# Kernel optimization log

Hardware: AMD Instinct MI355X
Metric: run time of the kernel (lower is better)

The kernel has to match this reference:

```python
import jax, jax.numpy as jnp
import numpy as np

B, CIN, COUT, H, W, K = 32, 256, 256, 64, 64, 3


def setup_inputs() -> dict:
    key = jax.random.key(0)
    k1, k2, k3 = jax.random.split(key, 3)
    x = jax.random.normal(k1, (B, CIN, H, W), dtype=jnp.float32)
    # kaiming_uniform_ with a=sqrt(5): bound = sqrt(6 / ((1 + a^2) * fan_in)) = sqrt(1/fan_in)
    fan_in = CIN * K * K
    bound = float(np.sqrt(1.0 / fan_in))
    weight = jax.random.uniform(k2, (COUT, CIN, K, K), dtype=jnp.float32,
                                minval=-bound, maxval=bound)
    bias = jax.random.normal(k3, (COUT,), dtype=jnp.float32)
    return {"x": x, "weight": weight, "bias": bias}


def reference(x, weight, bias):
    # CustomConvnd with kernel=3, stride=1, padding=1 (module doubles it, pad
    # helper splits around center -> 1 element each side, zero padding),
    # equivalent to a standard 2D cross-correlation like torch Conv2d.
    out = jax.lax.conv_general_dilated(
        x, weight,
        window_strides=(1, 1),
        padding=((1, 1), (1, 1)),
        dimension_numbers=("NCHW", "OIHW", "NCHW"),
    )
    return out + bias[None, :, None, None]
```

## Files before the change

kernel.cpp:

```cpp
#include <hip/hip_runtime.h>
#include <hip/hip_bf16.h>

typedef __attribute__((ext_vector_type(8))) short short8;
typedef __attribute__((ext_vector_type(4))) float floatx4;

#define BDIM 512

constexpr int kCIN = 256, kCOUT = 256, kH = 64, kW = 64;
constexpr int BK = 32;
constexpr int NCHUNK = kCIN / BK;
constexpr int XR = 4, XC = 66, NPIX = XR * XC;
constexpr int HW = kH * kW;

__device__ __forceinline__ int swz16(int row, int g) {
    return ((g ^ ((row >> 1) & 3)) << 4);
}

__device__ __forceinline__ unsigned short f2bf(float f) {
    unsigned u = __float_as_uint(f);
    u += 0x7fffu + ((u >> 16) & 1u);
    return (unsigned short)(u >> 16);
}

__global__ void wt_transform_kernel(const float* __restrict__ wsrc,
                                    unsigned short* __restrict__ wt) {
    int idx = blockIdx.x * 256 + threadIdx.x;
    if (idx >= 9 * 256 * 256) return;
    int ci = idx & 255;
    int co = (idx >> 8) & 255;
    int kk = idx >> 16;
    wt[idx] = f2bf(wsrc[(co * 256 + ci) * 9 + kk]);
}

__global__ __launch_bounds__(BDIM)
void conv3x3_mfma_kernel(const float* __restrict__ x,
                         const unsigned short* __restrict__ wt,
                         const float* __restrict__ bias,
                         float* __restrict__ out) {
    __shared__ __align__(16) char xs[NPIX * 64];
    __shared__ __align__(16) char ws[2][256 * 64];

    const int bid = blockIdx.x;
    const int b = bid >> 5;
    const int h0 = (bid & 31) * 2;

    const int tid = threadIdx.x;
    const int wv = tid >> 6;
    const int l = tid & 63;
    const int lo = l & 15;
    const int hi = l >> 4;
    const int co0w = (wv & 3) * 64;
    const int wpix = wv >> 2;

    const float* xb = x + (size_t)b * kCIN * HW;

    floatx4 acc[4][4] = {};

    for (int chunk = 0; chunk < NCHUNK; ++chunk) {
        const int ci0 = chunk * BK;

        for (int t = tid; t < NPIX * 4; t += BDIM) {
            int g = t / NPIX;
            int rem = t - g * NPIX;
            int r = rem / XC;
            int c = rem - r * XC;
            int ih = h0 - 1 + r;
            int iw = c - 1;
            float v[8];
            if ((unsigned)ih < (unsigned)kH && (unsigned)iw < (unsigned)kW) {
                const float* p = xb + (size_t)(ci0 + g * 8) * HW + ih * kW + iw;
                #pragma unroll
                for (int j = 0; j < 8; ++j) v[j] = p[(size_t)j * HW];
            } else {
                #pragma unroll
                for (int j = 0; j < 8; ++j) v[j] = 0.f;
            }
            union { short8 s8; unsigned short u[8]; } pk;
            #pragma unroll
            for (int j = 0; j < 8; ++j) pk.u[j] = f2bf(v[j]);
            int pix = r * XC + c;
            *(short8*)(xs + pix * 64 + swz16(pix, g)) = pk.s8;
        }
        {
            const unsigned short* wsrcp = wt + ci0;
            for (int t = tid; t < 1024; t += BDIM) {
                int co = t >> 2, g = t & 3;
                short8 v = *(const short8*)(wsrcp + co * 256 + g * 8);
                *(short8*)(ws[0] + co * 64 + swz16(co, g)) = v;
            }
        }
        __syncthreads();

        for (int kk = 0; kk < 9; ++kk) {
            if (kk < 8) {
                const unsigned short* wsrcp = wt + (size_t)(kk + 1) * 65536 + ci0;
                char* wbuf = ws[(kk + 1) & 1];
                for (int t = tid; t < 1024; t += BDIM) {
                    int co = t >> 2, g = t & 3;
                    short8 v = *(const short8*)(wsrcp + co * 256 + g * 8);
                    *(short8*)(wbuf + co * 64 + swz16(co, g)) = v;
                }
            }
            {
                const char* wbuf = ws[kk & 1];
                short8 a[4], bfr[4];
                #pragma unroll
                for (int i = 0; i < 4; ++i) {
                    int co = co0w + i * 16 + lo;
                    a[i] = *(const short8*)(wbuf + co * 64 + swz16(co, hi));
                }
                const int kh = kk / 3, kw = kk - kh * 3;
                const int r = wpix + kh;
                #pragma unroll
                for (int f = 0; f < 4; ++f) {
                    int pix = r * XC + f * 16 + lo + kw;
                    bfr[f] = *(const short8*)(xs + pix * 64 + swz16(pix, hi));
                }
                #pragma unroll
                for (int i = 0; i < 4; ++i) {
                    #pragma unroll
                    for (int f = 0; f < 4; ++f) {
                        acc[i][f] = __builtin_amdgcn_mfma_f32_16x16x32_bf16(
                            a[i], bfr[f], acc[i][f], 0, 0, 0);
                    }
                }
            }
            __syncthreads();
        }
    }

    const int h = h0 + wpix;
    float* op = out + (size_t)b * kCOUT * HW;
    #pragma unroll
    for (int i = 0; i < 4; ++i) {
        #pragma unroll
        for (int rg = 0; rg < 4; ++rg) {
            int co = co0w + i * 16 + hi * 4 + rg;
            float bv = bias[co];
            #pragma unroll
            for (int f = 0; f < 4; ++f) {
                int wcol = f * 16 + lo;
                op[((size_t)co * kH + h) * kW + wcol] = acc[i][f][rg] + bv;
            }
        }
    }
}

extern "C" void kernel_launch(void* const* d_in, const int* in_sizes, int n_in,
                              void* d_out, int out_size, void* d_ws, size_t ws_size,
                              hipStream_t stream) {
    const float* x    = (const float*)d_in[0];
    const float* wsrc = (const float*)d_in[1];
    const float* bias = (const float*)d_in[2];
    float* out = (float*)d_out;
    unsigned short* wt = (unsigned short*)d_ws;

    hipLaunchKernelGGL(wt_transform_kernel, dim3((9 * 256 * 256 + 255) / 256),
                       dim3(256), 0, stream, wsrc, wt);

    const int kB = 32;
    hipLaunchKernelGGL(conv3x3_mfma_kernel, dim3(kB * (kH / 2)), dim3(BDIM),
                       0, stream, x, wt, bias, out);
}
```

Measured before the change: 191.4 us.

## Enlarge conv tile to four rows, use 32x32 MFMA and async weight loads

Each block now computes four output rows instead of two, and each wave owns a 128-channel by 64-pixel tile built from 32x32x16 bf16 MFMAs instead of 16x16x32. The aim is to halve the weight traffic per output and raise MFMA work per LDS read. Weight staging switches to global_load_lds direct-to-LDS copies, flattened into one pipelined loop over chunk and tap, with launch bounds asking for two blocks per CU. The costs are a larger X halo tile, a heavier accumulator register footprint, and half as many blocks.

```diff
diff --git a/kernel.cpp b/kernel.cpp
--- a/kernel.cpp
+++ b/kernel.cpp
@@ -2,15 +2,17 @@
 #include <hip/hip_bf16.h>
 
 typedef __attribute__((ext_vector_type(8))) short short8;
-typedef __attribute__((ext_vector_type(4))) float floatx4;
+typedef __attribute__((ext_vector_type(16))) float floatx16;
 
 #define BDIM 512
 
 constexpr int kCIN = 256, kCOUT = 256, kH = 64, kW = 64;
 constexpr int BK = 32;
 constexpr int NCHUNK = kCIN / BK;
-constexpr int XR = 4, XC = 66, NPIX = XR * XC;
+constexpr int ROWS = 4;
+constexpr int XR = ROWS + 2, XC = 66, NPIX = XR * XC;
 constexpr int HW = kH * kW;
+constexpr int NSTEP = NCHUNK * 9;
 
 __device__ __forceinline__ int swz16(int row, int g) {
     return ((g ^ ((row >> 1) & 3)) << 4);
@@ -32,7 +34,7 @@
     wt[idx] = f2bf(wsrc[(co * 256 + ci) * 9 + kk]);
 }
 
-__global__ __launch_bounds__(BDIM)
+__global__ __launch_bounds__(BDIM, 2)
 void conv3x3_mfma_kernel(const float* __restrict__ x,
                          const unsigned short* __restrict__ wt,
                          const float* __restrict__ bias,
@@ -41,24 +43,40 @@
     __shared__ __align__(16) char ws[2][256 * 64];
 
     const int bid = blockIdx.x;
-    const int b = bid >> 5;
-    const int h0 = (bid & 31) * 2;
+    const int b  = bid >> 4;
+    const int h0 = (bid & 15) * ROWS;
 
     const int tid = threadIdx.x;
-    const int wv = tid >> 6;
-    const int l = tid & 63;
-    const int lo = l & 15;
-    const int hi = l >> 4;
-    const int co0w = (wv & 3) * 64;
-    const int wpix = wv >> 2;
+    const int wv  = tid >> 6;
+    const int l   = tid & 63;
+    const int l31 = l & 31;
+    const int hi2 = l >> 5;
+    const int cog  = (wv & 1) * 128;
+    const int wrow = wv >> 1;
 
     const float* xb = x + (size_t)b * kCIN * HW;
 
-    floatx4 acc[4][4] = {};
+    floatx16 acc[4][2] = {};
 
-    for (int chunk = 0; chunk < NCHUNK; ++chunk) {
+    auto stageW = [&](int st) {
+        int chunk = st / 9, kk = st - chunk * 9;
+        const unsigned short* wp = wt + (size_t)kk * 65536 + chunk * BK;
+        char* wbuf = ws[st & 1];
+        #pragma unroll
+        for (int it = 0; it < 2; ++it) {
+            int row0 = it * 128 + wv * 16;
+            int co = row0 + (l >> 2);
+            int g  = (l & 3) ^ ((co >> 1) & 3);
+            const unsigned short* src = wp + co * 256 + g * 8;
+            __builtin_amdgcn_global_load_lds(
+                (const __attribute__((address_space(1))) unsigned int*)src,
+                (__attribute__((address_space(3))) unsigned int*)(wbuf + row0 * 64),
+                16, 0, 0);
+        }
+    };
+
+    auto stageX = [&](int chunk) {
         const int ci0 = chunk * BK;
-
         for (int t = tid; t < NPIX * 4; t += BDIM) {
             int g = t / NPIX;
             int rem = t - g * NPIX;
@@ -81,66 +99,62 @@
             int pix = r * XC + c;
             *(short8*)(xs + pix * 64 + swz16(pix, g)) = pk.s8;
         }
-        {
-            const unsigned short* wsrcp = wt + ci0;
-            for (int t = tid; t < 1024; t += BDIM) {
-                int co = t >> 2, g = t & 3;
-                short8 v = *(const short8*)(wsrcp + co * 256 + g * 8);
-                *(short8*)(ws[0] + co * 64 + swz16(co, g)) = v;
+    };
+
+    stageX(0);
+    stageW(0);
+    __syncthreads();
+
+    for (int st = 0; st < NSTEP; ++st) {
+        const int chunk = st / 9;
+        const int kk = st - chunk * 9;
+        if (st < NSTEP - 1) stageW(st + 1);
+
+        const char* wbuf = ws[st & 1];
+        const int kh = kk / 3, kwo = kk - kh * 3;
+        const int r = wrow + kh;
+
+        short8 a[2][4], bfr[2][2];
+        #pragma unroll
+        for (int s = 0; s < 2; ++s) {
+            const int g = s * 2 + hi2;
+            #pragma unroll
+            for (int i = 0; i < 4; ++i) {
+                int co = cog + i * 32 + l31;
+                a[s][i] = *(const short8*)(wbuf + co * 64 + swz16(co, g));
+            }
+            #pragma unroll
+            for (int f = 0; f < 2; ++f) {
+                int pix = r * XC + f * 32 + l31 + kwo;
+                bfr[s][f] = *(const short8*)(xs + pix * 64 + swz16(pix, g));
             }
         }
+        #pragma unroll
+        for (int s = 0; s < 2; ++s)
+            #pragma unroll
+            for (int i = 0; i < 4; ++i)
+                #pragma unroll
+                for (int f = 0; f < 2; ++f)
+                    acc[i][f] = __builtin_amdgcn_mfma_f32_32x32x16_bf16(
+                        a[s][i], bfr[s][f], acc[i][f], 0, 0, 0);
         __syncthreads();
 
-        for (int kk = 0; kk < 9; ++kk) {
-            if (kk < 8) {
-                const unsigned short* wsrcp = wt + (size_t)(kk + 1) * 65536 + ci0;
-                char* wbuf = ws[(kk + 1) & 1];
-                for (int t = tid; t < 1024; t += BDIM) {
-                    int co = t >> 2, g = t & 3;
-                    short8 v = *(const short8*)(wsrcp + co * 256 + g * 8);
-                    *(short8*)(wbuf + co * 64 + swz16(co, g)) = v;
-                }
-            }
-            {
-                const char* wbuf = ws[kk & 1];
-                short8 a[4], bfr[4];
-                #pragma unroll
-                for (int i = 0; i < 4; ++i) {
-                    int co = co0w + i * 16 + lo;
-                    a[i] = *(const short8*)(wbuf + co * 64 + swz16(co, hi));
-                }
-                const int kh = kk / 3, kw = kk - kh * 3;
-                const int r = wpix + kh;
-                #pragma unroll
-                for (int f = 0; f < 4; ++f) {
-                    int pix = r * XC + f * 16 + lo + kw;
-                    bfr[f] = *(const short8*)(xs + pix * 64 + swz16(pix, hi));
-                }
-                #pragma unroll
-                for (int i = 0; i < 4; ++i) {
-                    #pragma unroll
-                    for (int f = 0; f < 4; ++f) {
-                        acc[i][f] = __builtin_amdgcn_mfma_f32_16x16x32_bf16(
-                            a[i], bfr[f], acc[i][f], 0, 0, 0);
-                    }
-                }
-            }
+        if (kk == 8 && st < NSTEP - 1) {
+            stageX(chunk + 1);
             __syncthreads();
         }
     }
 
-    const int h = h0 + wpix;
-    float* op = out + (size_t)b * kCOUT * HW;
+    float* op = out + (size_t)b * kCOUT * HW + (size_t)(h0 + wrow) * kW;
     #pragma unroll
     for (int i = 0; i < 4; ++i) {
         #pragma unroll
-        for (int rg = 0; rg < 4; ++rg) {
-            int co = co0w + i * 16 + hi * 4 + rg;
+        for (int rg = 0; rg < 16; ++rg) {
+            int co = cog + i * 32 + (rg & 3) + 8 * (rg >> 2) + 4 * hi2;
             float bv = bias[co];
             #pragma unroll
-            for (int f = 0; f < 4; ++f) {
-                int wcol = f * 16 + lo;
-                op[((size_t)co * kH + h) * kW + wcol] = acc[i][f][rg] + bv;
+            for (int f = 0; f < 2; ++f) {
+                op[(size_t)co * HW + f * 32 + l31] = acc[i][f][rg] + bv;
             }
         }
     }
@@ -158,7 +172,6 @@
     hipLaunchKernelGGL(wt_transform_kernel, dim3((9 * 256 * 256 + 255) / 256),
                        dim3(256), 0, stream, wsrc, wt);
 
-    const int kB = 32;
-    hipLaunchKernelGGL(conv3x3_mfma_kernel, dim3(kB * (kH / 2)), dim3(BDIM),
+    hipLaunchKernelGGL(conv3x3_mfma_kernel, dim3(32 * (kH / ROWS)), dim3(BDIM),
                        0, stream, x, wt, bias, out);
 }
```

Result: slower. 198.0 us (+3.5%).
